# Kernel tuning notes

Hardware: AMD Instinct MI355X
Metric: run time of the kernel (lower is better)

## Reference

```python
import jax, jax.numpy as jnp
import numpy as np

L = 8        # number of node layers in the DAG
D = 64       # width of every node layer
B = 262144   # batch
N_CONN = L * (L - 1) // 2  # 28 all-to-all forward connections


def setup_inputs() -> dict:
    key = jax.random.key(0)
    kx, kw, kb = jax.random.split(key, 3)
    x = jax.random.normal(kx, (B, D), dtype=jnp.float32)
    # connection weights, torch Linear convention: y = x @ W.T + b, W is [out, in]
    Ws = jax.random.normal(kw, (N_CONN, D, D), dtype=jnp.float32) * (1.0 / np.sqrt(D))
    bs = jax.random.normal(kb, (N_CONN, D), dtype=jnp.float32) * 0.1
    return {"x": x, "Ws": Ws, "bs": bs}


def reference(x, Ws, bs):
    # outputs[0] = input; outputs[1..L-1] start at zero and accumulate messages.
    outs = [x] + [jnp.zeros((x.shape[0], D), dtype=x.dtype) for _ in range(L - 1)]
    # Same iteration order as the torch double loop: source i ascending,
    # target offset i2 ascending; connection c maps layer i -> layer i+i2+1.
    c = 0
    for i in range(L):
        for i2 in range(L - 1 - i):
            j = i + i2 + 1
            outs[j] = outs[j] + jax.nn.relu(outs[i] @ Ws[c].T + bs[c])
            c += 1
    return outs[L - 1]
```

## Files before the change

### kernel.cpp

```cpp
#include <hip/hip_runtime.h>


#define DD 64
#define NCONN 28
#define THREADS 256
#define ROWS_PER_BLOCK 64
#define MAT_ELEMS 4096

typedef __bf16 bf16x8 __attribute__((ext_vector_type(8)));
typedef float f32x4 __attribute__((ext_vector_type(4)));
typedef unsigned short u16x8 __attribute__((ext_vector_type(8)));

__device__ constexpr int OFFS[7] = {0, 7, 13, 18, 22, 25, 27};
__device__ constexpr int CONN[28] = {0, 1,7, 2,8,13, 3,9,14,18, 4,10,15,19,22,
                                     5,11,16,20,23,25, 6,12,17,21,24,26,27};

__device__ __forceinline__ unsigned short f2bfu(float f) {
    return __builtin_bit_cast(unsigned short, (__bf16)f);
}

__device__ __forceinline__ f32x4 vmax4(f32x4 a, f32x4 b) {
#if __has_builtin(__builtin_elementwise_max)
    return __builtin_elementwise_max(a, b);
#else
    f32x4 r;
    r[0] = fmaxf(a[0], b[0]); r[1] = fmaxf(a[1], b[1]);
    r[2] = fmaxf(a[2], b[2]); r[3] = fmaxf(a[3], b[3]);
    return r;
#endif
}

__device__ __forceinline__ void gll16(const unsigned short* g, unsigned short* l) {
    __builtin_amdgcn_global_load_lds(
        (const __attribute__((address_space(1))) unsigned int*)g,
        (__attribute__((address_space(3))) unsigned int*)l, 16, 0, 0);
}

__device__ __forceinline__ void lds_barrier() {
    asm volatile("s_waitcnt lgkmcnt(0)" ::: "memory");
    __builtin_amdgcn_s_barrier();
    asm volatile("" ::: "memory");
}

__global__ void wconv_kernel(const float* __restrict__ w,
                             unsigned short* __restrict__ o) {
    int i = blockIdx.x * blockDim.x + threadIdx.x;
    if (i >= NCONN * 512) return;
    int conn = i >> 9;
    int within = i & 511;
    int r  = within >> 3;
    int k0 = (within & 7) << 3;
    const float* src = w + conn * MAT_ELEMS + r * DD + k0;
    float4 v0 = *reinterpret_cast<const float4*>(src);
    float4 v1 = *reinterpret_cast<const float4*>(src + 4);
    u16x8 d;
    d[0] = f2bfu(v0.x); d[1] = f2bfu(v0.y); d[2] = f2bfu(v0.z); d[3] = f2bfu(v0.w);
    d[4] = f2bfu(v1.x); d[5] = f2bfu(v1.y); d[6] = f2bfu(v1.z); d[7] = f2bfu(v1.w);
    *reinterpret_cast<u16x8*>(o + conn * MAT_ELEMS + r * DD + (k0 ^ ((r & 7) << 3))) = d;
}

template <bool GLL>
__global__ __launch_bounds__(THREADS, 3)
void dag_kernel(const float* __restrict__ x,
                const float* __restrict__ Wf,
                const unsigned short* __restrict__ Wimg,
                const float* __restrict__ bs,
                float* __restrict__ out) {
    __shared__ __align__(16) unsigned short ring[4 * MAT_ELEMS];
    __shared__ __align__(16) unsigned short sB[2 * 2048];
    __shared__ __align__(16) float sBias[NCONN * DD];

    const int tid  = threadIdx.x;
    const int lane = tid & 63;
    const int wv   = tid >> 6;
    const int pair = wv >> 1;
    const int h    = wv & 1;
    const int l15  = lane & 15;
    const int kg   = lane >> 4;

    const long rowbase = (long)blockIdx.x * ROWS_PER_BLOCK + pair * 32;

    for (int idx = tid; idx < NCONN * DD / 4; idx += THREADS)
        reinterpret_cast<float4*>(sBias)[idx] = reinterpret_cast<const float4*>(bs)[idx];

    bf16x8 afrag[7][2][2];
#pragma unroll
    for (int rt = 0; rt < 2; ++rt) {
        const float* xr = x + (rowbase + rt * 16 + l15) * DD;
#pragma unroll
        for (int s = 0; s < 2; ++s) {
            float4 v0 = *reinterpret_cast<const float4*>(xr + s * 32 + kg * 8);
            float4 v1 = *reinterpret_cast<const float4*>(xr + s * 32 + kg * 8 + 4);
            bf16x8 f;
            f[0] = (__bf16)v0.x; f[1] = (__bf16)v0.y; f[2] = (__bf16)v0.z; f[3] = (__bf16)v0.w;
            f[4] = (__bf16)v1.x; f[5] = (__bf16)v1.y; f[6] = (__bf16)v1.z; f[7] = (__bf16)v1.w;
            afrag[0][rt][s] = f;
        }
    }

    auto stage_gll = [&](int p) {
        const unsigned short* src = Wimg + CONN[p] * MAT_ELEMS + wv * 512 + lane * 8;
        unsigned short* dst = ring + (p & 3) * MAT_ELEMS + wv * 512;
#pragma unroll
        for (int hh = 0; hh < 2; ++hh)
            gll16(src + hh * 2048, dst + hh * 2048);
    };
    auto stage_direct = [&](int p) {
        const float* wp = Wf + CONN[p] * MAT_ELEMS;
#pragma unroll
        for (int hh = 0; hh < 2; ++hh) {
            const int e0 = hh * 2048 + tid * 8;
            float4 a0 = *reinterpret_cast<const float4*>(wp + e0);
            float4 a1 = *reinterpret_cast<const float4*>(wp + e0 + 4);
            u16x8 d;
            d[0] = f2bfu(a0.x); d[1] = f2bfu(a0.y); d[2] = f2bfu(a0.z); d[3] = f2bfu(a0.w);
            d[4] = f2bfu(a1.x); d[5] = f2bfu(a1.y); d[6] = f2bfu(a1.z); d[7] = f2bfu(a1.w);
            const int r = e0 >> 6, k0 = e0 & 63;
            *reinterpret_cast<u16x8*>(ring + (p & 3) * MAT_ELEMS +
                                      r * DD + (k0 ^ ((r & 7) << 3))) = d;
        }
    };

    if constexpr (GLL) { stage_gll(0); stage_gll(1); }
    __syncthreads();

    unsigned short* myPB = sB + pair * 2048;
    f32x4 acc[2][2];

#pragma unroll
    for (int j = 1; j <= 7; ++j) {
#pragma unroll
        for (int rt = 0; rt < 2; ++rt)
#pragma unroll
            for (int t = 0; t < 2; ++t) {
                acc[rt][t][0] = 0.f; acc[rt][t][1] = 0.f;
                acc[rt][t][2] = 0.f; acc[rt][t][3] = 0.f;
            }

#pragma unroll
        for (int i = 0; i < j; ++i) {
            const int p = j * (j - 1) / 2 + i;
            const int c = OFFS[i] + (j - i - 1);

            if constexpr (GLL) {
                if ((p & 1) == 0) {
                    if (p > 0) __syncthreads();
                    if (p + 2 < NCONN) { stage_gll(p + 2); stage_gll(p + 3); }
                }
            } else {
                __syncthreads();
                stage_direct(p);
                __syncthreads();
            }

            const unsigned short* wsl = ring + (p & 3) * MAT_ELEMS;
            __builtin_amdgcn_s_setprio(1);
#pragma unroll
            for (int t = 0; t < 2; ++t) {
                const int n  = h * 32 + t * 16 + l15;
                const int xo = (n & 7) << 3;
                u16x8 rw0 = *reinterpret_cast<const u16x8*>(wsl + n * DD + ((kg * 8) ^ xo));
                u16x8 rw1 = *reinterpret_cast<const u16x8*>(wsl + n * DD + ((32 + kg * 8) ^ xo));
                const float bv = sBias[c * DD + n];
                const f32x4 b4 = {bv, bv, bv, bv};
#pragma unroll
                for (int rt = 0; rt < 2; ++rt) {
                    f32x4 C = acc[rt][t];
                    C = __builtin_amdgcn_mfma_f32_16x16x32_bf16(
                            afrag[i][rt][0], __builtin_bit_cast(bf16x8, rw0), C, 0, 0, 0);
                    C = __builtin_amdgcn_mfma_f32_16x16x32_bf16(
                            afrag[i][rt][1], __builtin_bit_cast(bf16x8, rw1), C, 0, 0, 0);
                    acc[rt][t] = vmax4(C + b4, acc[rt][t]);
                }
            }
            __builtin_amdgcn_s_setprio(0);
        }

        if (j < 7) {
#pragma unroll
            for (int rt = 0; rt < 2; ++rt)
#pragma unroll
                for (int t = 0; t < 2; ++t) {
                    const int f = h * 32 + t * 16 + l15;
#pragma unroll
                    for (int q = 0; q < 4; ++q) {
                        const int mr = rt * 16 + kg * 4 + q;
                        myPB[mr * DD + (f ^ ((mr & 7) << 3))] = f2bfu(acc[rt][t][q]);
                    }
                }
            lds_barrier();
#pragma unroll
            for (int rt = 0; rt < 2; ++rt)
#pragma unroll
                for (int s = 0; s < 2; ++s) {
                    u16x8 ra = *reinterpret_cast<const u16x8*>(
                        &myPB[(rt * 16 + l15) * DD + ((s * 32 + kg * 8) ^ ((l15 & 7) << 3))]);
                    afrag[j][rt][s] = __builtin_bit_cast(bf16x8, ra);
                }
            lds_barrier();
        } else {
            float* orow = out + rowbase * DD;
#pragma unroll
            for (int rt = 0; rt < 2; ++rt)
#pragma unroll
                for (int t = 0; t < 2; ++t)
#pragma unroll
                    for (int q = 0; q < 4; ++q)
                        orow[(rt * 16 + kg * 4 + q) * DD + h * 32 + t * 16 + l15] =
                            acc[rt][t][q];
        }
    }
}

extern "C" void kernel_launch(void* const* d_in, const int* in_sizes, int n_in,
                              void* d_out, int out_size, void* d_ws, size_t ws_size,
                              hipStream_t stream) {
    const float* x  = (const float*)d_in[0];
    const float* Ws = (const float*)d_in[1];
    const float* bs = (const float*)d_in[2];
    float* out = (float*)d_out;

    const int nrows = in_sizes[0] / DD;
    const int grid  = nrows / ROWS_PER_BLOCK;

    const size_t wbf_bytes = (size_t)NCONN * MAT_ELEMS * sizeof(unsigned short);
    if (ws_size >= wbf_bytes) {
        unsigned short* wbf = (unsigned short*)d_ws;
        wconv_kernel<<<(NCONN * 512 + 255) / 256, 256, 0, stream>>>(Ws, wbf);
        dag_kernel<true><<<grid, THREADS, 0, stream>>>(x, Ws, wbf, bs, out);
    } else {
        dag_kernel<false><<<grid, THREADS, 0, stream>>>(x, Ws, nullptr, bs, out);
    }
}
```

Baseline: 102.4 us.

## Double-buffer activation exchange and prefetch biases into registers, dropping LDS barriers

Removes the shared-memory bias table and instead prefetches per-connection bias values from global memory into registers, alongside the weight staging. The per-layer activation handoff now uses a double-buffered LDS region, so the two lds_barrier calls per layer go away. Fragments are read back lazily at the first connection of the next layer, after an existing __syncthreads. This cuts barrier count and LDS footprint, but relies on the existing weight-ring barriers for correctness and adds register pressure.

```diff
diff --git a/kernel.cpp b/kernel.cpp
--- a/kernel.cpp
+++ b/kernel.cpp
@@ -34,12 +34,6 @@
     __builtin_amdgcn_global_load_lds(
         (const __attribute__((address_space(1))) unsigned int*)g,
         (__attribute__((address_space(3))) unsigned int*)l, 16, 0, 0);
-}
-
-__device__ __forceinline__ void lds_barrier() {
-    asm volatile("s_waitcnt lgkmcnt(0)" ::: "memory");
-    __builtin_amdgcn_s_barrier();
-    asm volatile("" ::: "memory");
 }
 
 __global__ void wconv_kernel(const float* __restrict__ w,
@@ -67,8 +61,7 @@
                 const float* __restrict__ bs,
                 float* __restrict__ out) {
     __shared__ __align__(16) unsigned short ring[4 * MAT_ELEMS];
-    __shared__ __align__(16) unsigned short sB[2 * 2048];
-    __shared__ __align__(16) float sBias[NCONN * DD];
+    __shared__ __align__(16) unsigned short sB[2 * 2 * 2048];
 
     const int tid  = threadIdx.x;
     const int lane = tid & 63;
@@ -80,9 +73,6 @@
 
     const long rowbase = (long)blockIdx.x * ROWS_PER_BLOCK + pair * 32;
 
-    for (int idx = tid; idx < NCONN * DD / 4; idx += THREADS)
-        reinterpret_cast<float4*>(sBias)[idx] = reinterpret_cast<const float4*>(bs)[idx];
-
     bf16x8 afrag[7][2][2];
 #pragma unroll
     for (int rt = 0; rt < 2; ++rt) {
@@ -97,6 +87,13 @@
             afrag[0][rt][s] = f;
         }
     }
+
+    float breg[2][2][2];
+    auto loadBias = [&](int p) {
+        const float* bp = bs + CONN[p] * DD + h * 32 + l15;
+        float* b = breg[(p >> 1) & 1][p & 1];
+        b[0] = bp[0]; b[1] = bp[16];
+    };
 
     auto stage_gll = [&](int p) {
         const unsigned short* src = Wimg + CONN[p] * MAT_ELEMS + wv * 512 + lane * 8;
@@ -121,14 +118,16 @@
         }
     };
 
+    loadBias(0); loadBias(1);
     if constexpr (GLL) { stage_gll(0); stage_gll(1); }
     __syncthreads();
 
-    unsigned short* myPB = sB + pair * 2048;
+    unsigned short* myPB = sB + pair * 4096;
     f32x4 acc[2][2];
 
 #pragma unroll
     for (int j = 1; j <= 7; ++j) {
+        const int T = j * (j - 1) / 2;
 #pragma unroll
         for (int rt = 0; rt < 2; ++rt)
 #pragma unroll
@@ -139,21 +138,36 @@
 
 #pragma unroll
         for (int i = 0; i < j; ++i) {
-            const int p = j * (j - 1) / 2 + i;
-            const int c = OFFS[i] + (j - i - 1);
+            const int p = T + i;
 
             if constexpr (GLL) {
                 if ((p & 1) == 0) {
                     if (p > 0) __syncthreads();
+                    if (p + 2 < NCONN) { loadBias(p + 2); loadBias(p + 3); }
                     if (p + 2 < NCONN) { stage_gll(p + 2); stage_gll(p + 3); }
                 }
             } else {
                 __syncthreads();
                 stage_direct(p);
+                loadBias(p);
                 __syncthreads();
             }
 
+            if (j >= 2 && p == T + (GLL ? (T & 1) : 0)) {
+                const unsigned short* rb = myPB + ((j - 1) & 1) * 2048;
+#pragma unroll
+                for (int rt = 0; rt < 2; ++rt)
+#pragma unroll
+                    for (int s = 0; s < 2; ++s) {
+                        u16x8 ra = *reinterpret_cast<const u16x8*>(
+                            &rb[(rt * 16 + l15) * DD +
+                                ((s * 32 + kg * 8) ^ ((l15 & 7) << 3))]);
+                        afrag[j - 1][rt][s] = __builtin_bit_cast(bf16x8, ra);
+                    }
+            }
+
             const unsigned short* wsl = ring + (p & 3) * MAT_ELEMS;
+            const float* bv = breg[(p >> 1) & 1][p & 1];
             __builtin_amdgcn_s_setprio(1);
 #pragma unroll
             for (int t = 0; t < 2; ++t) {
@@ -161,8 +175,7 @@
                 const int xo = (n & 7) << 3;
                 u16x8 rw0 = *reinterpret_cast<const u16x8*>(wsl + n * DD + ((kg * 8) ^ xo));
                 u16x8 rw1 = *reinterpret_cast<const u16x8*>(wsl + n * DD + ((32 + kg * 8) ^ xo));
-                const float bv = sBias[c * DD + n];
-                const f32x4 b4 = {bv, bv, bv, bv};
+                const f32x4 b4 = {bv[t], bv[t], bv[t], bv[t]};
 #pragma unroll
                 for (int rt = 0; rt < 2; ++rt) {
                     f32x4 C = acc[rt][t];
@@ -177,6 +190,7 @@
         }
 
         if (j < 7) {
+            unsigned short* wb = myPB + (j & 1) * 2048;
 #pragma unroll
             for (int rt = 0; rt < 2; ++rt)
 #pragma unroll
@@ -185,19 +199,9 @@
 #pragma unroll
                     for (int q = 0; q < 4; ++q) {
                         const int mr = rt * 16 + kg * 4 + q;
-                        myPB[mr * DD + (f ^ ((mr & 7) << 3))] = f2bfu(acc[rt][t][q]);
+                        wb[mr * DD + (f ^ ((mr & 7) << 3))] = f2bfu(acc[rt][t][q]);
                     }
                 }
-            lds_barrier();
-#pragma unroll
-            for (int rt = 0; rt < 2; ++rt)
-#pragma unroll
-                for (int s = 0; s < 2; ++s) {
-                    u16x8 ra = *reinterpret_cast<const u16x8*>(
-                        &myPB[(rt * 16 + l15) * DD + ((s * 32 + kg * 8) ^ ((l15 & 7) << 3))]);
-                    afrag[j][rt][s] = __builtin_bit_cast(bf16x8, ra);
-                }
-            lds_barrier();
         } else {
             float* orow = out + rowbase * DD;
 #pragma unroll
```

New measurement: 122.2 us. +19.3%, slower.
